# Performance work log

Measured on AMD Instinct MI355X. Metric: run time of the kernel, lower is better.

## Reference

```python
import jax, jax.numpy as jnp
import numpy as np
import math

B, T, C, H, L, V = 16, 512, 1024, 16, 4, 32000
D = C // H


def setup_inputs() -> dict:
    key = jax.random.key(0)
    ks = jax.random.split(key, 10)
    X = jax.random.randint(ks[0], (B, T), 0, V)
    S = jax.random.bernoulli(ks[1], 0.5, (B, T)).astype(jnp.int32)
    # I + S must equal 1 everywhere, else get_attn_mask fully masks a row -> NaN softmax
    I = (1 - S).astype(jnp.float32)
    s = 0.02
    emb_table = jax.random.normal(ks[2], (V + 1, C), jnp.float32) * s
    pos_emb = jax.random.normal(ks[3], (T, C), jnp.float32) * s
    qkv_w = jax.random.normal(ks[4], (L, 3 * C, C), jnp.float32) * s
    out_w = jax.random.normal(ks[5], (L, C, C), jnp.float32) * s
    ffn_w1 = jax.random.normal(ks[6], (L, C, C), jnp.float32) * s
    ffn_b1 = jnp.zeros((L, C), jnp.float32)
    ffn_w2 = jax.random.normal(ks[7], (L, C, C), jnp.float32) * s
    ffn_b2 = jnp.zeros((L, C), jnp.float32)
    return dict(X=X, I=I, S=S, emb_table=emb_table, pos_emb=pos_emb,
                qkv_w=qkv_w, out_w=out_w, ffn_w1=ffn_w1, ffn_b1=ffn_b1,
                ffn_w2=ffn_w2, ffn_b2=ffn_b2)


def _forward(X, I, S, emb_table, pos_emb, qkv_w, out_w, ffn_w1, ffn_b1, ffn_w2, ffn_b2):
    # token_to_embeddings: unobserved (S==0) tokens remapped to sentinel index V
    Xm = X * S + (1 - S) * V                      # [B,T]
    x = emb_table[Xm] + pos_emb[None]             # [B,T,C]
    # additive mask from outer product of validity flags m = I + S
    m = I + S.astype(I.dtype)                     # [B,T]
    prod = m[:, :, None] * m[:, None, :]          # [B,T,T]
    bias = jnp.where(prod == 1.0, 0.0, -jnp.inf)[:, None]  # [B,1,T,T]
    scale = 1.0 / math.sqrt(D)
    for i in range(L):
        wq, wk, wv = qkv_w[i, :C], qkv_w[i, C:2 * C], qkv_w[i, 2 * C:]
        q = (x @ wq.T).reshape(B, T, H, D)
        k = (x @ wk.T).reshape(B, T, H, D)
        v = (x @ wv.T).reshape(B, T, H, D)
        scores = jnp.einsum('bqhd,bkhd->bhqk', q * scale, k) + bias
        attn = jax.nn.softmax(scores, axis=-1)
        o = jnp.einsum('bhqk,bkhd->bqhd', attn, v).reshape(B, T, C)
        x = o @ out_w[i].T + x                    # out projection + residual
        h = jax.nn.relu(x @ ffn_w1[i].T + ffn_b1[i])
        x = x + (h @ ffn_w2[i].T + ffn_b2[i])
    # readout: bmm(x^T, I) -> [B,C]
    return jnp.einsum('btc,bt->bc', x, I)


def reference(X, I, S, emb_table, pos_emb, qkv_w, out_w, ffn_w1, ffn_b1, ffn_w2, ffn_b2):
    return _forward(X, I, S, emb_table, pos_emb, qkv_w, out_w,
                    ffn_w1, ffn_b1, ffn_w2, ffn_b2)
```

## Files before the change

### kernel.cpp

```cpp
#include <hip/hip_runtime.h>
#include <stdint.h>

#define LAYERS 4
#define BB 16
#define TT 512
#define CC 1024
#define HH 16
#define DD 64
#define VV 32000
#define MM (BB*TT)

typedef __attribute__((ext_vector_type(8))) short bf16x8;
typedef __attribute__((ext_vector_type(4))) float f32x4;
typedef __attribute__((ext_vector_type(16))) float f32x16;

__device__ __forceinline__ unsigned short f2b(float f) {
  union { float f; unsigned int u; } v; v.f = f;
  unsigned int r = v.u + 0x7FFFu + ((v.u >> 16) & 1u);
  return (unsigned short)(r >> 16);
}
__device__ __forceinline__ float blo(unsigned int u) {
  union { unsigned int x; float f; } v; v.x = u << 16; return v.f;
}
__device__ __forceinline__ float bhi(unsigned int u) {
  union { unsigned int x; float f; } v; v.x = u & 0xFFFF0000u; return v.f;
}
__device__ __forceinline__ uint32_t pkbf(float lo, float hi) {
  uint32_t d; asm("v_cvt_pk_bf16_f32 %0, %1, %2" : "=v"(d) : "v"(lo), "v"(hi)); return d;
}
__device__ __forceinline__ float ex2(float x) {
  float r; asm("v_exp_f32 %0, %1" : "=v"(r) : "v"(x)); return r;
}
__device__ __forceinline__ void gload16(const unsigned short* g, const unsigned short* lds) {
  __builtin_amdgcn_global_load_lds((const __attribute__((address_space(1))) void*)g,
                                   (__attribute__((address_space(3))) void*)lds, 16, 0, 0);
}

__global__ __launch_bounds__(256) void cvt4_kernel(
    const float* __restrict__ a, const float* __restrict__ b,
    const float* __restrict__ c, const float* __restrict__ d,
    unsigned short* __restrict__ wa, unsigned short* __restrict__ wb,
    unsigned short* __restrict__ wc, unsigned short* __restrict__ wd) {
  const int nA = LAYERS * 3 * CC * CC / 4;
  const int nR = LAYERS * CC * CC / 4;
  int i = blockIdx.x * 256 + threadIdx.x;
  const float* src; unsigned short* dst; int off;
  if (i < nA)               { src = a; dst = wa; off = i; }
  else if (i < nA + nR)     { src = b; dst = wb; off = i - nA; }
  else if (i < nA + 2 * nR) { src = c; dst = wc; off = i - nA - nR; }
  else                      { src = d; dst = wd; off = i - nA - 2 * nR; }
  float4 v = ((const float4*)src)[off];
  ushort4 o; o.x = f2b(v.x); o.y = f2b(v.y); o.z = f2b(v.z); o.w = f2b(v.w);
  ((ushort4*)dst)[off] = o;
}

__global__ __launch_bounds__(256) void embed_kernel(const int* __restrict__ X, const int* __restrict__ S,
    const float* __restrict__ emb, const float* __restrict__ pos,
    float* __restrict__ x, unsigned short* __restrict__ xb) {
  int bt = blockIdx.x; int tid = threadIdx.x;
  int t = bt & (TT - 1);
  int tok = S[bt] ? X[bt] : VV;
  float4 e = ((const float4*)(emb + (size_t)tok * CC))[tid];
  float4 p = ((const float4*)(pos + (size_t)t * CC))[tid];
  float4 r; r.x = e.x + p.x; r.y = e.y + p.y; r.z = e.z + p.z; r.w = e.w + p.w;
  ((float4*)(x + (size_t)bt * CC))[tid] = r;
  ushort4 ub; ub.x = f2b(r.x); ub.y = f2b(r.y); ub.z = f2b(r.z); ub.w = f2b(r.w);
  ((ushort4*)(xb + (size_t)bt * CC))[tid] = ub;
}

template<int EPI, int BM>
__global__ __launch_bounds__(512, 4) void gemm8_kernel(
    const unsigned short* __restrict__ A,
    const unsigned short* __restrict__ W,
    float* __restrict__ xres,
    unsigned short* __restrict__ outb,
    const float* __restrict__ bias,
    int N, int nbx) {
  constexpr int NA = BM / 128;
  constexpr int MI = BM / 64;
  constexpr int BUFS = (BM + 128) * 32;
  extern __shared__ unsigned short lds[];
  const int K = 1024;
  const int tid = threadIdx.x;
  const int wv = tid >> 6, ln = tid & 63;
  const int g = ln >> 4, rr = ln & 15;
  const int wm = wv >> 1, wn = wv & 1;

  const int nwg = gridDim.x;
  const int bid = blockIdx.x;
  const int swz = (bid & 7) * (nwg >> 3) + (bid >> 3);
  const int by = swz / nbx, bx = swz - by * nbx;
  const int brow = by * BM, bcol = bx * 128;

  const unsigned short* asrc[NA];
  #pragma unroll
  for (int rd = 0; rd < NA; ++rd) {
    int p = rd * 512 + tid;
    int row = p >> 2, gg = p & 3;
    asrc[rd] = A + (size_t)(brow + row) * K + (gg ^ ((row >> 1) & 3)) * 8;
  }
  const unsigned short* bsrc;
  {
    int row = tid >> 2, gg = tid & 3;
    bsrc = W + (size_t)(bcol + row) * K + (gg ^ ((row >> 1) & 3)) * 8;
  }

  auto stage = [&](int tile, int buf) {
    unsigned short* Aba = lds + buf * BUFS;
    unsigned short* Bba = Aba + BM * 32;
    int ko = tile * 32;
    #pragma unroll
    for (int rd = 0; rd < NA; ++rd)
      gload16(asrc[rd] + ko, Aba + (rd * 512 + wv * 64) * 8);
    gload16(bsrc + ko, Bba + (wv * 64) * 8);
  };

  f32x4 acc[MI][4];
  #pragma unroll
  for (int i = 0; i < MI; ++i)
    #pragma unroll
    for (int j = 0; j < 4; ++j)
      acc[i][j] = (f32x4){0.f, 0.f, 0.f, 0.f};

  stage(0, 0);

  const int chx = (g ^ ((rr >> 1) & 3)) * 8;
  for (int t = 0; t < 32; ++t) {
    if (t < 31) {
      stage(t + 1, (t + 1) & 1);
      asm volatile("s_waitcnt vmcnt(%0)" :: "i"(NA + 1) : "memory");
    } else {
      asm volatile("s_waitcnt vmcnt(0)" ::: "memory");
    }
    __builtin_amdgcn_s_barrier();
    __builtin_amdgcn_sched_barrier(0);

    const unsigned short* Aba = lds + (t & 1) * BUFS;
    const unsigned short* Bba = Aba + BM * 32;
    bf16x8 av[MI], bv[4];
    #pragma unroll
    for (int i = 0; i < MI; ++i)
      av[i] = *(const bf16x8*)(Aba + (wm * (BM / 4) + i * 16 + rr) * 32 + chx);
    #pragma unroll
    for (int j = 0; j < 4; ++j)
      bv[j] = *(const bf16x8*)(Bba + (wn * 64 + j * 16 + rr) * 32 + chx);

    __builtin_amdgcn_s_setprio(1);
    #pragma unroll
    for (int i = 0; i < MI; ++i)
      #pragma unroll
      for (int j = 0; j < 4; ++j)
        acc[i][j] = __builtin_amdgcn_mfma_f32_16x16x32_bf16(av[i], bv[j], acc[i][j], 0, 0, 0);
    __builtin_amdgcn_s_setprio(0);
    __builtin_amdgcn_sched_barrier(0);
    __builtin_amdgcn_s_barrier();
  }

  #pragma unroll
  for (int i = 0; i < MI; ++i) {
    #pragma unroll
    for (int j = 0; j < 4; ++j) {
      #pragma unroll
      for (int q = 0; q < 4; ++q) {
        int rowg = brow + wm * (BM / 4) + i * 16 + g * 4 + q;
        int colg = bcol + wn * 64 + j * 16 + rr;
        size_t off = (size_t)rowg * N + colg;
        float vacc = acc[i][j][q];
        if (EPI == 0) {
          outb[off] = f2b(vacc);
        } else if (EPI == 1) {
          float nx = xres[off] + vacc;
          xres[off] = nx; outb[off] = f2b(nx);
        } else if (EPI == 2) {
          float hv = vacc + bias[colg];
          hv = hv > 0.f ? hv : 0.f;
          outb[off] = f2b(hv);
        } else {
          float nx = xres[off] + vacc + bias[colg];
          xres[off] = nx; outb[off] = f2b(nx);
        }
      }
    }
  }
}

template<int E>
__device__ __forceinline__ bf16x8 buildP(const f32x16& p) {
  uint32_t a = pkbf(p[E + 0], p[E + 1]);
  uint32_t b = pkbf(p[E + 4], p[E + 5]);
  uint32_t c = pkbf(p[E + 2], p[E + 3]);
  uint32_t d = pkbf(p[E + 6], p[E + 7]);
  asm("v_permlane32_swap_b32 %0, %1" : "+v"(a), "+v"(b));
  asm("v_permlane32_swap_b32 %0, %1" : "+v"(c), "+v"(d));
  union { uint32_t u[4]; bf16x8 v; } r;
  r.u[0] = a; r.u[1] = c; r.u[2] = b; r.u[3] = d;
  return r.v;
}

__global__ __launch_bounds__(256) void attn_kernel(const unsigned short* __restrict__ qkv,
                                                   unsigned short* __restrict__ ob) {
  __shared__ unsigned short Kl[2][64 * 64];
  __shared__ unsigned short Vt[2][64 * 64];
  const int tid = threadIdx.x;
  const int wv = tid >> 6, ln = tid & 63;
  const int lq = ln & 31, hi = ln >> 5;
  const int qt = blockIdx.x >> 8, bh = blockIdx.x & 255;
  const int b = bh >> 4, h = bh & 15;
  const int qrow = qt * 128 + wv * 32 + lq;
  const size_t rowQ = (size_t)(b * TT + qrow) * 3072 + h * 64;

  const float cs = 0.125f * 1.44269504f;
  bf16x8 qf[4];
  #pragma unroll
  for (int t = 0; t < 4; ++t) {
    uint4 u = *(const uint4*)(qkv + rowQ + t * 16 + hi * 8);
    uint32_t w[4] = {u.x, u.y, u.z, u.w};
    union { uint32_t u4[4]; bf16x8 v; } cv;
    #pragma unroll
    for (int j = 0; j < 4; ++j) cv.u4[j] = pkbf(blo(w[j]) * cs, bhi(w[j]) * cs);
    qf[t] = cv.v;
  }

  auto stageK = [&](int i, int p) {
    #pragma unroll
    for (int r = 0; r < 2; ++r) {
      int ch = r * 256 + tid;
      int k = ch >> 3, cc = ch & 7;
      int sg = (k & 7) ^ (k >> 3);
      const unsigned short* gs = qkv + (size_t)(b * TT + i * 64 + k) * 3072 + 1024 + h * 64 + ((cc ^ sg) << 3);
      gload16(gs, &Kl[p][(size_t)(r * 256 + wv * 64) * 8]);
    }
  };
  auto loadV = [&](int i, uint4& g1, uint4& g2) {
    int cc = tid & 7, kp = tid >> 3;
    const unsigned short* gv = qkv + (size_t)(b * TT + i * 64 + kp * 2) * 3072 + 2048 + h * 64 + cc * 8;
    g1 = *(const uint4*)gv;
    g2 = *(const uint4*)(gv + 3072);
  };
  auto writeVt = [&](int p, uint4 g1, uint4 g2) {
    int cc = tid & 7, k = (tid >> 3) * 2;
    uint32_t w1[4] = {g1.x, g1.y, g1.z, g1.w}, w2[4] = {g2.x, g2.y, g2.z, g2.w};
    #pragma unroll
    for (int j = 0; j < 8; ++j) {
      int d = cc * 8 + j;
      uint32_t dw = (j & 1) ? ((w1[j >> 1] >> 16) | (w2[j >> 1] & 0xFFFF0000u))
                            : ((w1[j >> 1] & 0xFFFFu) | (w2[j >> 1] << 16));
      int sg = (d & 7) ^ (d >> 3);
      *(uint32_t*)(&Vt[p][d * 64 + (k ^ (sg << 3))]) = dw;
    }
  };

  f32x16 o0 = {}, o1 = {};
  float mrun = -3.0e38f, lsum = 0.f;

  uint4 vg1, vg2;
  stageK(0, 0);
  loadV(0, vg1, vg2);
  writeVt(0, vg1, vg2);
  asm volatile("s_waitcnt lgkmcnt(0)" ::: "memory");
  __builtin_amdgcn_s_barrier();

  for (int i = 0; i < 8; ++i) {
    const int p = i & 1;
    if (i < 7) { stageK(i + 1, p ^ 1); loadV(i + 1, vg1, vg2); }

    f32x16 s0 = {}, s1 = {};
    __builtin_amdgcn_s_setprio(1);
    #pragma unroll
    for (int t = 0; t < 4; ++t) {
      int r0 = lq, r1 = 32 + lq;
      bf16x8 a0 = *(const bf16x8*)(&Kl[p][r0 * 64 + ((((t << 1) | hi) ^ ((r0 & 7) ^ (r0 >> 3))) << 3)]);
      bf16x8 a1 = *(const bf16x8*)(&Kl[p][r1 * 64 + ((((t << 1) | hi) ^ ((r1 & 7) ^ (r1 >> 3))) << 3)]);
      s0 = __builtin_amdgcn_mfma_f32_32x32x16_bf16(a0, qf[t], s0, 0, 0, 0);
      s1 = __builtin_amdgcn_mfma_f32_32x32x16_bf16(a1, qf[t], s1, 0, 0, 0);
    }
    __builtin_amdgcn_s_setprio(0);

    float m8[8];
    #pragma unroll
    for (int r = 0; r < 8; ++r)
      m8[r] = fmaxf(fmaxf(s0[r], s0[r + 8]), fmaxf(s1[r], s1[r + 8]));
    #pragma unroll
    for (int st = 4; st > 0; st >>= 1)
      #pragma unroll
      for (int r = 0; r < st; ++r)
        m8[r] = fmaxf(m8[r], m8[r + st]);
    float mx = fmaxf(m8[0], __shfl_xor(m8[0], 32));

    if (!__all(mx - mrun <= 8.0f)) {
      float mnew = fmaxf(mrun, mx);
      float cf = ex2(mrun - mnew);
      lsum *= cf;
      #pragma unroll
      for (int r = 0; r < 16; ++r) { o0[r] *= cf; o1[r] *= cf; }
      mrun = mnew;
    }
    #pragma unroll
    for (int r = 0; r < 16; ++r) {
      s0[r] = ex2(s0[r] - mrun);
      s1[r] = ex2(s1[r] - mrun);
      lsum += s0[r] + s1[r];
    }

    bf16x8 pf0 = buildP<0>(s0);
    bf16x8 pf1 = buildP<8>(s0);
    bf16x8 pf2 = buildP<0>(s1);
    bf16x8 pf3 = buildP<8>(s1);

    if (i < 7) writeVt(p ^ 1, vg1, vg2);

    __builtin_amdgcn_s_setprio(1);
    #pragma unroll
    for (int t = 0; t < 4; ++t) {
      bf16x8 pf = (t == 0) ? pf0 : (t == 1) ? pf1 : (t == 2) ? pf2 : pf3;
      int d0 = lq, d1 = 32 + lq;
      bf16x8 v0 = *(const bf16x8*)(&Vt[p][d0 * 64 + ((((t << 1) | hi) ^ ((d0 & 7) ^ (d0 >> 3))) << 3)]);
      bf16x8 v1 = *(const bf16x8*)(&Vt[p][d1 * 64 + ((((t << 1) | hi) ^ ((d1 & 7) ^ (d1 >> 3))) << 3)]);
      o0 = __builtin_amdgcn_mfma_f32_32x32x16_bf16(v0, pf, o0, 0, 0, 0);
      o1 = __builtin_amdgcn_mfma_f32_32x32x16_bf16(v1, pf, o1, 0, 0, 0);
    }
    __builtin_amdgcn_s_setprio(0);

    asm volatile("s_waitcnt lgkmcnt(0)" ::: "memory");
    __builtin_amdgcn_sched_barrier(0);
    __builtin_amdgcn_s_barrier();
  }

  lsum += __shfl_xor(lsum, 32);
  float inv = 1.f / lsum;
  size_t orow = (size_t)(b * TT + qrow) * CC + h * 64;
  #pragma unroll
  for (int md = 0; md < 2; ++md) {
    #pragma unroll
    for (int rq = 0; rq < 4; ++rq) {
      int d0 = md * 32 + rq * 8 + hi * 4;
      float e0 = (md ? o1[rq * 4 + 0] : o0[rq * 4 + 0]) * inv;
      float e1 = (md ? o1[rq * 4 + 1] : o0[rq * 4 + 1]) * inv;
      float e2 = (md ? o1[rq * 4 + 2] : o0[rq * 4 + 2]) * inv;
      float e3 = (md ? o1[rq * 4 + 3] : o0[rq * 4 + 3]) * inv;
      uint2 st; st.x = pkbf(e0, e1); st.y = pkbf(e2, e3);
      *(uint2*)(ob + orow + d0) = st;
    }
  }
}

__global__ __launch_bounds__(256) void final_kernel(const float* __restrict__ x,
                                                    const float* __restrict__ I,
                                                    float* __restrict__ out) {
  int b = blockIdx.x >> 2;
  int c = ((blockIdx.x & 3) << 8) + threadIdx.x;
  float acc = 0.f;
  const float* xp = x + (size_t)b * TT * CC + c;
  const float* Ip = I + (size_t)b * TT;
  for (int t = 0; t < TT; ++t) acc = fmaf(xp[(size_t)t * CC], Ip[t], acc);
  out[b * CC + c] = acc;
}

extern "C" void kernel_launch(void* const* d_in, const int* in_sizes, int n_in,
                              void* d_out, int out_size, void* d_ws, size_t ws_size,
                              hipStream_t stream) {
  const int*   X      = (const int*)d_in[0];
  const float* I      = (const float*)d_in[1];
  const int*   S      = (const int*)d_in[2];
  const float* emb    = (const float*)d_in[3];
  const float* pos    = (const float*)d_in[4];
  const float* qkv_w  = (const float*)d_in[5];
  const float* out_w  = (const float*)d_in[6];
  const float* ffn_w1 = (const float*)d_in[7];
  const float* ffn_b1 = (const float*)d_in[8];
  const float* ffn_w2 = (const float*)d_in[9];
  const float* ffn_b2 = (const float*)d_in[10];
  float* out = (float*)d_out;

  char* ws = (char*)d_ws;
  size_t off = 0;
  auto walloc = [&](size_t bytes) { char* p = ws + off; off += (bytes + 255) & ~(size_t)255; return p; };
  unsigned short* wqkv = (unsigned short*)walloc((size_t)LAYERS * 3 * CC * CC * 2);
  unsigned short* wo   = (unsigned short*)walloc((size_t)LAYERS * CC * CC * 2);
  unsigned short* w1   = (unsigned short*)walloc((size_t)LAYERS * CC * CC * 2);
  unsigned short* w2   = (unsigned short*)walloc((size_t)LAYERS * CC * CC * 2);
  float*          x    = (float*)walloc((size_t)MM * CC * 4);
  unsigned short* xb   = (unsigned short*)walloc((size_t)MM * CC * 2);
  unsigned short* qkvb = (unsigned short*)walloc((size_t)MM * 3 * CC * 2);
  unsigned short* obuf = (unsigned short*)walloc((size_t)MM * CC * 2);
  unsigned short* hbuf = (unsigned short*)walloc((size_t)MM * CC * 2);
  if (off > ws_size) return;

  const int nCvt = (LAYERS * 3 * CC * CC + 3 * LAYERS * CC * CC) / 4;
  cvt4_kernel<<<(nCvt + 255) / 256, 256, 0, stream>>>(qkv_w, out_w, ffn_w1, ffn_w2,
                                                      wqkv, wo, w1, w2);

  embed_kernel<<<MM, 256, 0, stream>>>(X, S, emb, pos, x, xb);

  const size_t lds128 = 2 * (128 + 128) * 32 * 2;
  for (int l = 0; l < LAYERS; ++l) {
    gemm8_kernel<0, 128><<<(MM / 128) * (3 * CC / 128), 512, lds128, stream>>>(
        xb, wqkv + (size_t)l * 3 * CC * CC, nullptr, qkvb, nullptr, 3 * CC, 3 * CC / 128);
    attn_kernel<<<4 * 256, 256, 0, stream>>>(qkvb, obuf);
    gemm8_kernel<1, 128><<<(MM / 128) * (CC / 128), 512, lds128, stream>>>(
        obuf, wo + (size_t)l * CC * CC, x, xb, nullptr, CC, CC / 128);
    gemm8_kernel<2, 128><<<(MM / 128) * (CC / 128), 512, lds128, stream>>>(
        xb, w1 + (size_t)l * CC * CC, nullptr, hbuf, ffn_b1 + l * CC, CC, CC / 128);
    gemm8_kernel<3, 128><<<(MM / 128) * (CC / 128), 512, lds128, stream>>>(
        hbuf, w2 + (size_t)l * CC * CC, x, xb, ffn_b2 + l * CC, CC, CC / 128);
  }

  final_kernel<<<BB * 4, 256, 0, stream>>>(x, I, out);
}
```

Baseline: 817.3 us.

## Add 256x256-tile pipelined GEMM kernel for QKV projection

Adds a new GEMM kernel with 256x256 output tiles, a 64-wide K step split into two 32-wide halves, and double-buffered LDS (128 KB) fed by direct global-to-LDS loads. MFMA work is interleaved with the next tile's loads, using explicit waitcnt, scheduling barriers and setprio. It replaces the 128x128 kernel only for the QKV projection. The larger tile raises operand reuse and cuts global traffic, at the cost of lower occupancy (2 blocks per CU at most, probably fewer given the LDS size) and scalar, uncoalesced epilogue stores.

Result: no change. 810.3 us (-0.8%).

```diff
diff --git a/kernel.cpp b/kernel.cpp
--- a/kernel.cpp
+++ b/kernel.cpp
@@ -66,6 +66,122 @@
   ((float4*)(x + (size_t)bt * CC))[tid] = r;
   ushort4 ub; ub.x = f2b(r.x); ub.y = f2b(r.y); ub.z = f2b(r.z); ub.w = f2b(r.w);
   ((ushort4*)(xb + (size_t)bt * CC))[tid] = ub;
+}
+
+__global__ __launch_bounds__(512, 2) void gemm10_kernel(
+    const unsigned short* __restrict__ A,
+    const unsigned short* __restrict__ W,
+    unsigned short* __restrict__ outb,
+    int N, int nbx) {
+  extern __shared__ unsigned short lds[];
+  const int K = 1024;
+  const int tid = threadIdx.x;
+  const int wv = tid >> 6, ln = tid & 63;
+  const int g = ln >> 4, rr = ln & 15;
+  const int wm = wv >> 2, wn = wv & 3;
+
+  const int nwg = gridDim.x;
+  const int bid = blockIdx.x;
+  const int swz = (bid & 7) * (nwg >> 3) + (bid >> 3);
+  const int by = swz / nbx, bx = swz - by * nbx;
+  const int brow = by * 256, bcol = bx * 256;
+
+  const unsigned short* asrc[2];
+  const unsigned short* bsrc[2];
+  #pragma unroll
+  for (int rd = 0; rd < 2; ++rd) {
+    int row = rd * 128 + (tid >> 2);
+    int gg = tid & 3;
+    asrc[rd] = A + (size_t)(brow + row) * K + (gg ^ ((row >> 1) & 3)) * 8;
+    bsrc[rd] = W + (size_t)(bcol + row) * K + (gg ^ ((row >> 1) & 3)) * 8;
+  }
+
+  auto reg = [&](int par, int kk, int ab) -> unsigned short* {
+    return lds + (((((par << 1) | kk) << 1) | ab) * 8192);
+  };
+  auto stageKK = [&](int tile, int kk) {
+    const int par = tile & 1;
+    const int ko = tile * 64 + kk * 32;
+    unsigned short* Ad = reg(par, kk, 0);
+    unsigned short* Bd = reg(par, kk, 1);
+    #pragma unroll
+    for (int rd = 0; rd < 2; ++rd) {
+      gload16(asrc[rd] + ko, Ad + (rd * 512 + wv * 64) * 8);
+      gload16(bsrc[rd] + ko, Bd + (rd * 512 + wv * 64) * 8);
+    }
+  };
+
+  f32x4 acc[8][4];
+  #pragma unroll
+  for (int i = 0; i < 8; ++i)
+    #pragma unroll
+    for (int j = 0; j < 4; ++j)
+      acc[i][j] = (f32x4){0.f, 0.f, 0.f, 0.f};
+
+  const int chx = (g ^ ((rr >> 1) & 3)) * 8;
+
+  stageKK(0, 0);
+  stageKK(0, 1);
+  asm volatile("s_waitcnt vmcnt(4)" ::: "memory");
+  __builtin_amdgcn_s_barrier();
+
+#define PHASE(MQ, KK, STG, GT) { \
+    const unsigned short* Ar = reg(p, KK, 0); \
+    const unsigned short* Br = reg(p, KK, 1); \
+    bf16x8 av[4], bv[4]; \
+    _Pragma("unroll") \
+    for (int i = 0; i < 4; ++i) \
+      av[i] = *(const bf16x8*)(Ar + (wm * 128 + MQ * 64 + i * 16 + rr) * 32 + chx); \
+    _Pragma("unroll") \
+    for (int j = 0; j < 4; ++j) \
+      bv[j] = *(const bf16x8*)(Br + (wn * 64 + j * 16 + rr) * 32 + chx); \
+    STG; \
+    __builtin_amdgcn_s_barrier(); \
+    asm volatile("s_waitcnt lgkmcnt(0)" ::: "memory"); \
+    __builtin_amdgcn_sched_barrier(0); \
+    __builtin_amdgcn_s_setprio(1); \
+    _Pragma("unroll") \
+    for (int i = 0; i < 4; ++i) \
+      _Pragma("unroll") \
+      for (int j = 0; j < 4; ++j) \
+        acc[MQ * 4 + i][j] = __builtin_amdgcn_mfma_f32_16x16x32_bf16(av[i], bv[j], acc[MQ * 4 + i][j], 0, 0, 0); \
+    __builtin_amdgcn_s_setprio(0); \
+    GT; \
+    __builtin_amdgcn_sched_barrier(0); \
+    __builtin_amdgcn_s_barrier(); \
+  }
+
+  for (int t = 0; t < 16; ++t) {
+    const int p = t & 1;
+    if (t < 15) {
+      PHASE(0, 0, stageKK(t + 1, 0), )
+      PHASE(1, 0, , asm volatile("s_waitcnt vmcnt(4)" ::: "memory"))
+      PHASE(0, 1, stageKK(t + 1, 1), )
+      PHASE(1, 1, , asm volatile("s_waitcnt vmcnt(4)" ::: "memory"))
+    } else {
+      PHASE(0, 0, , )
+      PHASE(1, 0, , asm volatile("s_waitcnt vmcnt(0)" ::: "memory"))
+      PHASE(0, 1, , )
+      PHASE(1, 1, , )
+    }
+  }
+#undef PHASE
+
+  #pragma unroll
+  for (int mq = 0; mq < 2; ++mq) {
+    #pragma unroll
+    for (int i = 0; i < 4; ++i) {
+      #pragma unroll
+      for (int j = 0; j < 4; ++j) {
+        #pragma unroll
+        for (int q = 0; q < 4; ++q) {
+          int rowg = brow + wm * 128 + mq * 64 + i * 16 + g * 4 + q;
+          int colg = bcol + wn * 64 + j * 16 + rr;
+          outb[(size_t)rowg * N + colg] = f2b(acc[mq * 4 + i][j][q]);
+        }
+      }
+    }
+  }
 }
 
 template<int EPI, int BM>
@@ -392,10 +508,11 @@
 
   embed_kernel<<<MM, 256, 0, stream>>>(X, S, emb, pos, x, xb);
 
+  const size_t lds10  = 128 * 1024;
   const size_t lds128 = 2 * (128 + 128) * 32 * 2;
   for (int l = 0; l < LAYERS; ++l) {
-    gemm8_kernel<0, 128><<<(MM / 128) * (3 * CC / 128), 512, lds128, stream>>>(
-        xb, wqkv + (size_t)l * 3 * CC * CC, nullptr, qkvb, nullptr, 3 * CC, 3 * CC / 128);
+    gemm10_kernel<<<(MM / 256) * (3 * CC / 256), 512, lds10, stream>>>(
+        xb, wqkv + (size_t)l * 3 * CC * CC, qkvb, 3 * CC, 3 * CC / 256);
     attn_kernel<<<4 * 256, 256, 0, stream>>>(qkvb, obuf);
     gemm8_kernel<1, 128><<<(MM / 128) * (CC / 128), 512, lds128, stream>>>(
         obuf, wo + (size_t)l * CC * CC, x, xb, nullptr, CC, CC / 128);
```
